# Kernel optimization log

Measured on AMD Instinct MI355X. Metric: run time of the kernel, lower is better.

## Reference

```python
import jax, jax.numpy as jnp
import numpy as np


def _global_field(gi, W1, b1, W2, b2, W3, b3):
    # define_mlp([256,256], global_dim+3, hid_dim, 'ReLU', layer_norm=False)
    h = jax.nn.relu(gi @ W1 + b1)
    h = jax.nn.relu(h @ W2 + b2)
    return h @ W3 + b3  # [..., hid_dim]


def setup_inputs() -> dict:
    key = jax.random.key(0)
    ks = jax.random.split(key, 16)
    B, T, R, P = 4, 4, 512, 32
    G, H = 256, 128
    gin = G + 3  # global_n_freqs is None -> global_in_dim = global_dim + 3
    s = lambda d: 1.0 / np.sqrt(d)
    return {
        'x': jax.random.normal(ks[0], (B, T, R, P, 3), jnp.float32),
        'ray_dir': jax.random.normal(ks[1], (B, T, R, 1, 3), jnp.float32),
        'mask': jax.random.randint(ks[2], (B, T, R, P, 1), 0, 2) == 1,
        'global_feat': jax.random.normal(ks[3], (B, G), jnp.float32),
        'offset': jax.random.normal(ks[4], (B, 3), jnp.float32),
        'local_feat': jax.random.normal(ks[5], (B, T, R, P, H), jnp.float32),
        'W1': jax.random.normal(ks[6], (gin, 256), jnp.float32) * s(gin),
        'b1': jnp.zeros((256,), jnp.float32),
        'W2': jax.random.normal(ks[7], (256, 256), jnp.float32) * s(256),
        'b2': jnp.zeros((256,), jnp.float32),
        'W3': jax.random.normal(ks[8], (256, H), jnp.float32) * s(256),
        'b3': jnp.zeros((H,), jnp.float32),
        'Ws': jax.random.normal(ks[9], (H, 1), jnp.float32) * s(H),
        'bs': jnp.zeros((1,), jnp.float32),
        'Wc': jax.random.normal(ks[10], (H + 3, 3), jnp.float32) * s(H + 3),
        'bc': jnp.zeros((3,), jnp.float32),
    }


def reference(x, ray_dir, mask, global_feat, offset, local_feat,
              W1, b1, W2, b2, W3, b3, Ws, bs, Wc, bc):
    B, T, R, P, _ = x.shape
    m = mask  # [B,T,R,P,1] bool
    # get_global_feat: subtract per-batch offset, gather global_feat per point, concat
    xo = x - offset[:, None, None, None, :]                      # [B,T,R,P,3]
    g = jnp.broadcast_to(global_feat[:, None, None, None, :],
                         (B, T, R, P, global_feat.shape[-1]))    # [B,T,R,P,G]
    gi = jnp.concatenate((g, xo), axis=-1)                       # [B,T,R,P,G+3]
    gfeat = _global_field(gi, W1, b1, W2, b2, W3, b3)            # [B,T,R,P,H]
    # aggregate_shape=False path: feat = aggregated local feat + global feat
    feat = local_feat + gfeat
    # get_shape + shape_act (nerf=True -> softplus(x - 1)), scatter_shape zeros outside mask
    shape = jax.nn.softplus((feat @ Ws + bs) - 1.0)              # [B,T,R,P,1]
    # get_channels on feat + ray_dir, then sigmoid
    rd = jnp.broadcast_to(ray_dir, (B, T, R, P, 3))
    ch = jax.nn.sigmoid(jnp.concatenate((feat, rd), axis=-1) @ Wc + bc)  # [B,T,R,P,3]
    out = jnp.concatenate((shape, ch), axis=-1)
    # dense masked-scatter: valid points keep values, invalid are zero
    return jnp.where(m, out, 0.0)
```

## Files before the change

### kernel.cpp

```cpp
#include <hip/hip_runtime.h>

typedef __attribute__((ext_vector_type(8))) _Float16 f16x8;
typedef __attribute__((ext_vector_type(4))) _Float16 f16x4;
typedef __attribute__((ext_vector_type(4))) float f32x4;

#define SOFF 32768
#define LDS_BYTES (32768 + 4096)
#define NPTS 262144

__device__ inline unsigned swz_h(unsigned row, unsigned colbyte){
  return row*512u + (colbyte ^ ((row & 7u) << 4));
}

__device__ inline f16x8 cvt8(f32x4 a, f32x4 b){
  f16x8 r;
  #pragma unroll
  for (int i = 0; i < 4; ++i){ r[i] = (_Float16)a[i]; r[4+i] = (_Float16)b[i]; }
  return r;
}

__global__ void prep_all(const float* __restrict__ gf, const float* __restrict__ off,
                         const float* __restrict__ W1, const float* __restrict__ b1,
                         const float* __restrict__ W2,
                         const float* __restrict__ W3, const float* __restrict__ b3,
                         const float* __restrict__ Ws, const float* __restrict__ bs,
                         const float* __restrict__ Wc, const float* __restrict__ bc,
                         _Float16* __restrict__ w2t, _Float16* __restrict__ w1h,
                         _Float16* __restrict__ base1h,
                         _Float16* __restrict__ whd, _Float16* __restrict__ wlf,
                         float* __restrict__ hcon, int* __restrict__ counter){
  const int blk = blockIdx.x, tid = threadIdx.x;
  if (blk < 256){
    int e = blk*256 + tid;
    int s = e >> 13, r = e & 8191, n = r >> 5, kk = r & 31;
    w2t[e] = (_Float16)W2[(s*32 + kk)*256 + n];
    if (e < 768){
      int d = e >> 8, j = e & 255;
      w1h[e] = (_Float16)W1[(256 + d)*256 + j];
    }
  } else if (blk < 260){
    int b = blk - 256, j = tid;
    float acc = b1[j];
    for (int k = 0; k < 256; ++k) acc += gf[b*256 + k] * W1[k*256 + j];
    for (int d = 0; d < 3; ++d)  acc -= off[b*3 + d] * W1[(256 + d)*256 + j];
    base1h[b*256 + j] = (_Float16)acc;
  } else {
    int k = tid;
    float s0 = 0.f, s1 = 0.f, s2 = 0.f, s3 = 0.f;
    for (int j = 0; j < 128; ++j){
      float w3 = W3[k*128 + j];
      s0 += w3 * Ws[j];
      s1 += w3 * Wc[j*3 + 0];
      s2 += w3 * Wc[j*3 + 1];
      s3 += w3 * Wc[j*3 + 2];
    }
    int base = (k >> 5)*512 + (k & 31);
    whd[base + 0*32] = (_Float16)s0;
    whd[base + 1*32] = (_Float16)s1;
    whd[base + 2*32] = (_Float16)s2;
    whd[base + 3*32] = (_Float16)s3;
    for (int o = 4; o < 16; ++o) whd[base + o*32] = (_Float16)0.f;
    if (k < 128){
      int bl = (k >> 5)*512 + (k & 31);
      wlf[bl + 0*32] = (_Float16)Ws[k];
      wlf[bl + 1*32] = (_Float16)Wc[k*3 + 0];
      wlf[bl + 2*32] = (_Float16)Wc[k*3 + 1];
      wlf[bl + 3*32] = (_Float16)Wc[k*3 + 2];
      for (int o = 4; o < 16; ++o) wlf[bl + o*32] = (_Float16)0.f;
    }
    if (k == 0){
      float c0 = bs[0], c1 = bc[0], c2 = bc[1], c3 = bc[2];
      for (int j = 0; j < 128; ++j){
        float bj = b3[j];
        c0 += bj * Ws[j];
        c1 += bj * Wc[j*3 + 0];
        c2 += bj * Wc[j*3 + 1];
        c3 += bj * Wc[j*3 + 2];
      }
      hcon[0] = c0; hcon[1] = c1; hcon[2] = c2; hcon[3] = c3;
      *counter = 0;
    }
  }
}

__global__ void compact_mask(const int* __restrict__ mk, int* __restrict__ idx,
                             int* __restrict__ counter, float* __restrict__ out){
  __shared__ int woff[16];
  __shared__ int sbase;
  const int tid = threadIdx.x;
  const int i = blockIdx.x*1024 + tid;
  const int lane = tid & 63, w = tid >> 6;
  int m = (mk[i] != 0);
  unsigned long long bal = __ballot(m);
  if (lane == 0) woff[w] = __popcll(bal);
  __syncthreads();
  if (tid == 0){
    int tot = 0;
    #pragma unroll
    for (int k = 0; k < 16; ++k){ int c = woff[k]; woff[k] = tot; tot += c; }
    sbase = atomicAdd(counter, tot);
  }
  __syncthreads();
  if (m){
    int off = __popcll(bal & ((1ull << lane) - 1ull));
    idx[sbase + woff[w] + off] = i;
  } else {
    *(f32x4*)(out + (size_t)i*4) = (f32x4)0.f;
  }
}

__global__ __launch_bounds__(256, 4) void field_main(
    const float* __restrict__ x, const float* __restrict__ rdv,
    const float* __restrict__ lf, const float* __restrict__ b2v,
    const _Float16* __restrict__ base1h, const _Float16* __restrict__ w1h,
    const _Float16* __restrict__ w2t, const _Float16* __restrict__ whd,
    const _Float16* __restrict__ wlf, const float* __restrict__ hcon,
    const float* __restrict__ Wc, const int* __restrict__ idx,
    const int* __restrict__ nvp, float* __restrict__ out)
{
  const int nv = *nvp;
  const int t0 = blockIdx.x * 64;
  if (t0 >= nv) return;
  const bool full = (t0 + 64 <= nv);

  __shared__ char lds[LDS_BYTES];
  const int tid = threadIdx.x;
  const int wid = tid >> 6, lane = tid & 63;
  const int arow = lane & 15, kgrp = lane >> 4;

  int pi_e = 0; float r0 = 0.f, r1 = 0.f, r2 = 0.f;
  if (tid < 64){
    int ii = t0 + tid; if (ii >= nv) ii = nv - 1;
    pi_e = idx[ii];
    const float* rp = rdv + (pi_e >> 5)*3;
    r0 = rp[0]; r1 = rp[1]; r2 = rp[2];
  }

  const int cw = wid * 64;

  {
    const int j0 = (tid & 31) * 8;
    const int mb = (tid >> 5) * 8;
    f16x8 w0  = *(const f16x8*)(w1h +   0 + j0);
    f16x8 w1v = *(const f16x8*)(w1h + 256 + j0);
    f16x8 w2v = *(const f16x8*)(w1h + 512 + j0);
    const f16x8 z8 = (f16x8)(_Float16)0;
    int pidx[8];
    if (full){
      int4 a = *(const int4*)(idx + t0 + mb);
      int4 b4 = *(const int4*)(idx + t0 + mb + 4);
      pidx[0]=a.x; pidx[1]=a.y; pidx[2]=a.z; pidx[3]=a.w;
      pidx[4]=b4.x; pidx[5]=b4.y; pidx[6]=b4.z; pidx[7]=b4.w;
    } else {
      #pragma unroll
      for (int m = 0; m < 8; ++m){
        int ii = t0 + mb + m; if (ii >= nv) ii = nv - 1;
        pidx[m] = idx[ii];
      }
    }
    #pragma unroll
    for (int m = 0; m < 8; ++m){
      int pi = pidx[m];
      int b  = pi >> 16;
      f16x8 bh = *(const f16x8*)(base1h + b*256 + j0);
      const float* xp = x + (size_t)pi*3;
      _Float16 X0 = (_Float16)xp[0];
      _Float16 X1 = (_Float16)xp[1];
      _Float16 X2 = (_Float16)xp[2];
      f16x8 t = bh;
      t += w0  * X0;
      t += w1v * X1;
      t += w2v * X2;
      t = __builtin_elementwise_max(t, z8);
      *(f16x8*)(lds + swz_h(mb + m, j0*2)) = t;
    }
  }
  __syncthreads();

  f32x4 acc[16];
  #pragma unroll
  for (int c = 0; c < 4; ++c){
    f32x4 bb = *(const f32x4*)(b2v + cw + c*16 + kgrp*4);
    #pragma unroll
    for (int r = 0; r < 4; ++r) acc[r*4+c] = bb;
  }
  #pragma unroll 2
  for (int s = 0; s < 8; ++s){
    f16x8 af[4], bf[4];
    #pragma unroll
    for (int r = 0; r < 4; ++r)
      af[r] = *(const f16x8*)(lds + swz_h(r*16 + arow, s*64 + kgrp*16));
    #pragma unroll
    for (int c = 0; c < 4; ++c)
      bf[c] = *(const f16x8*)(w2t + s*8192 + (cw + c*16 + arow)*32 + kgrp*8);
    __builtin_amdgcn_s_setprio(1);
    #pragma unroll
    for (int r = 0; r < 4; ++r)
      #pragma unroll
      for (int c = 0; c < 4; ++c)
        acc[r*4+c] = __builtin_amdgcn_mfma_f32_16x16x32_f16(bf[c], af[r], acc[r*4+c], 0, 0, 0);
    __builtin_amdgcn_s_setprio(0);
  }

  f32x4 lfa[4], lfb[4];
  #pragma unroll
  for (int c = 0; c < 4; ++c){
    int ii = t0 + c*16 + arow;
    if (!full && ii >= nv) ii = nv - 1;
    int pic = idx[ii];
    const float* lp = lf + (size_t)pic*128 + wid*32 + kgrp*8;
    lfa[c] = *(const f32x4*)lp;
    lfb[c] = *(const f32x4*)(lp + 4);
  }
  __syncthreads();

  #pragma unroll
  for (int r = 0; r < 4; ++r)
    #pragma unroll
    for (int c = 0; c < 4; ++c){
      int row = r*16 + arow;
      int colbyte = (cw + c*16 + kgrp*4) * 2;
      f16x4 v;
      #pragma unroll
      for (int j = 0; j < 4; ++j) v[j] = (_Float16)fmaxf(acc[r*4+c][j], 0.f);
      *(f16x4*)(lds + swz_h(row, colbyte)) = v;
    }

  f32x4 acc4h[4];
  #pragma unroll
  for (int c = 0; c < 4; ++c)
    #pragma unroll
    for (int j = 0; j < 4; ++j)
      acc4h[c][j] = (wid == 0 && kgrp == 0) ? hcon[j] : 0.f;

  #pragma unroll
  for (int s = 0; s < 2; ++s){
    f16x8 ah = *(const f16x8*)(whd + (wid*2 + s)*512 + arow*32 + kgrp*8);
    #pragma unroll
    for (int c = 0; c < 4; ++c){
      f16x8 bh2 = *(const f16x8*)(lds + swz_h(c*16 + arow, (cw + s*32 + kgrp*8)*2));
      acc4h[c] = __builtin_amdgcn_mfma_f32_16x16x32_f16(ah, bh2, acc4h[c], 0, 0, 0);
    }
  }
  {
    f16x8 afl = *(const f16x8*)(wlf + wid*512 + arow*32 + kgrp*8);
    #pragma unroll
    for (int c = 0; c < 4; ++c)
      acc4h[c] = __builtin_amdgcn_mfma_f32_16x16x32_f16(afl, cvt8(lfa[c], lfb[c]), acc4h[c], 0, 0, 0);
  }
  if (kgrp == 0){
    #pragma unroll
    for (int c = 0; c < 4; ++c)
      *(f32x4*)(lds + SOFF + wid*1024 + (c*16 + arow)*16) = acc4h[c];
  }
  __syncthreads();

  if (tid < 64 && t0 + tid < nv){
    f32x4 v = *(const f32x4*)(lds + SOFF + 0*1024 + tid*16);
    #pragma unroll
    for (int w = 1; w < 4; ++w)
      v += *(const f32x4*)(lds + SOFF + w*1024 + tid*16);
    float ps = v[0] - 1.0f;
    float shape = (ps > 20.f) ? ps : log1pf(expf(ps));
    float c0 = v[1] + r0*Wc[128*3+0] + r1*Wc[129*3+0] + r2*Wc[130*3+0];
    float c1 = v[2] + r0*Wc[128*3+1] + r1*Wc[129*3+1] + r2*Wc[130*3+1];
    float c2 = v[3] + r0*Wc[128*3+2] + r1*Wc[129*3+2] + r2*Wc[130*3+2];
    f32x4 o;
    o[0] = shape;
    o[1] = 1.f/(1.f + expf(-c0));
    o[2] = 1.f/(1.f + expf(-c1));
    o[3] = 1.f/(1.f + expf(-c2));
    *(f32x4*)(out + (size_t)pi_e*4) = o;
  }
}

extern "C" void kernel_launch(void* const* d_in, const int* in_sizes, int n_in,
                              void* d_out, int out_size, void* d_ws, size_t ws_size,
                              hipStream_t stream){
  const float* x   = (const float*)d_in[0];
  const float* rd  = (const float*)d_in[1];
  const int*   mk  = (const int*)d_in[2];
  const float* gf  = (const float*)d_in[3];
  const float* off = (const float*)d_in[4];
  const float* lf  = (const float*)d_in[5];
  const float* W1  = (const float*)d_in[6];
  const float* b1  = (const float*)d_in[7];
  const float* W2  = (const float*)d_in[8];
  const float* b2  = (const float*)d_in[9];
  const float* W3  = (const float*)d_in[10];
  const float* b3  = (const float*)d_in[11];
  const float* Ws  = (const float*)d_in[12];
  const float* bs  = (const float*)d_in[13];
  const float* Wc  = (const float*)d_in[14];
  const float* bc  = (const float*)d_in[15];

  char* ws = (char*)d_ws;
  _Float16* base1h = (_Float16*)(ws + 0);
  _Float16* w1h    = (_Float16*)(ws + 2048);
  _Float16* w2t    = (_Float16*)(ws + 4096);
  _Float16* whd    = (_Float16*)(ws + 135168);
  _Float16* wlf    = (_Float16*)(ws + 143360);
  float*    hcon   = (float*)   (ws + 147456);
  int*      counter= (int*)     (ws + 147472);
  int*      idx    = (int*)     (ws + 147520);

  prep_all<<<261, 256, 0, stream>>>(gf, off, W1, b1, W2, W3, b3, Ws, bs, Wc, bc,
                                    w2t, w1h, base1h, whd, wlf, hcon, counter);
  compact_mask<<<NPTS/1024, 1024, 0, stream>>>(mk, idx, counter, (float*)d_out);
  field_main<<<NPTS/64, 256, 0, stream>>>(x, rd, lf, b2,
                                          base1h, w1h, w2t, whd, wlf, hcon, Wc,
                                          idx, counter, (float*)d_out);
}
```

Before: 60.77 us.

## Pack compacted point coords as fp16 with index during mask compaction

```diff
diff --git a/kernel.cpp b/kernel.cpp
--- a/kernel.cpp
+++ b/kernel.cpp
@@ -3,6 +3,7 @@
 typedef __attribute__((ext_vector_type(8))) _Float16 f16x8;
 typedef __attribute__((ext_vector_type(4))) _Float16 f16x4;
 typedef __attribute__((ext_vector_type(4))) float f32x4;
+typedef __attribute__((ext_vector_type(4))) unsigned short u16x4;
 
 #define SOFF 32768
 #define LDS_BYTES (32768 + 4096)
@@ -17,6 +18,14 @@
   #pragma unroll
   for (int i = 0; i < 4; ++i){ r[i] = (_Float16)a[i]; r[4+i] = (_Float16)b[i]; }
   return r;
+}
+
+__device__ inline unsigned short f16bits(float f){
+  _Float16 h = (_Float16)f;
+  return *(unsigned short*)&h;
+}
+__device__ inline _Float16 bits16(unsigned short u){
+  return *(_Float16*)&u;
 }
 
 __global__ void prep_all(const float* __restrict__ gf, const float* __restrict__ off,
@@ -30,16 +39,22 @@
                          _Float16* __restrict__ whd, _Float16* __restrict__ wlf,
                          float* __restrict__ hcon, int* __restrict__ counter){
   const int blk = blockIdx.x, tid = threadIdx.x;
-  if (blk < 256){
-    int e = blk*256 + tid;
-    int s = e >> 13, r = e & 8191, n = r >> 5, kk = r & 31;
-    w2t[e] = (_Float16)W2[(s*32 + kk)*256 + n];
-    if (e < 768){
+  if (blk < 64){
+    #pragma unroll
+    for (int k = 0; k < 4; ++k){
+      int e = blk*1024 + k*256 + tid;
+      int s = e >> 13, r = e & 8191, n = r >> 5, kk = r & 31;
+      w2t[e] = (_Float16)W2[(s*32 + kk)*256 + n];
+    }
+  } else if (blk == 64){
+    #pragma unroll
+    for (int k = 0; k < 3; ++k){
+      int e = k*256 + tid;
       int d = e >> 8, j = e & 255;
       w1h[e] = (_Float16)W1[(256 + d)*256 + j];
     }
-  } else if (blk < 260){
-    int b = blk - 256, j = tid;
+  } else if (blk < 69){
+    int b = blk - 65, j = tid;
     float acc = b1[j];
     for (int k = 0; k < 256; ++k) acc += gf[b*256 + k] * W1[k*256 + j];
     for (int d = 0; d < 3; ++d)  acc -= off[b*3 + d] * W1[(256 + d)*256 + j];
@@ -83,7 +98,8 @@
   }
 }
 
-__global__ void compact_mask(const int* __restrict__ mk, int* __restrict__ idx,
+__global__ void compact_mask(const int* __restrict__ mk, const float* __restrict__ x,
+                             u16x4* __restrict__ px8, unsigned char* __restrict__ pib,
                              int* __restrict__ counter, float* __restrict__ out){
   __shared__ int woff[16];
   __shared__ int sbase;
@@ -103,25 +119,32 @@
   __syncthreads();
   if (m){
     int off = __popcll(bal & ((1ull << lane) - 1ull));
-    idx[sbase + woff[w] + off] = i;
+    int slot = sbase + woff[w] + off;
+    u16x4 r;
+    r[0] = f16bits(x[i*3 + 0]);
+    r[1] = f16bits(x[i*3 + 1]);
+    r[2] = f16bits(x[i*3 + 2]);
+    r[3] = (unsigned short)(i & 0xFFFF);
+    px8[slot] = r;
+    pib[slot] = (unsigned char)(i >> 16);
   } else {
     *(f32x4*)(out + (size_t)i*4) = (f32x4)0.f;
   }
 }
 
 __global__ __launch_bounds__(256, 4) void field_main(
-    const float* __restrict__ x, const float* __restrict__ rdv,
+    const float* __restrict__ rdv,
     const float* __restrict__ lf, const float* __restrict__ b2v,
     const _Float16* __restrict__ base1h, const _Float16* __restrict__ w1h,
     const _Float16* __restrict__ w2t, const _Float16* __restrict__ whd,
     const _Float16* __restrict__ wlf, const float* __restrict__ hcon,
-    const float* __restrict__ Wc, const int* __restrict__ idx,
+    const float* __restrict__ Wc, const u16x4* __restrict__ px8,
+    const unsigned char* __restrict__ pib,
     const int* __restrict__ nvp, float* __restrict__ out)
 {
   const int nv = *nvp;
   const int t0 = blockIdx.x * 64;
   if (t0 >= nv) return;
-  const bool full = (t0 + 64 <= nv);
 
   __shared__ char lds[LDS_BYTES];
   const int tid = threadIdx.x;
@@ -130,8 +153,8 @@
 
   int pi_e = 0; float r0 = 0.f, r1 = 0.f, r2 = 0.f;
   if (tid < 64){
-    int ii = t0 + tid; if (ii >= nv) ii = nv - 1;
-    pi_e = idx[ii];
+    u16x4 px = px8[t0 + tid];
+    pi_e = ((pib[t0 + tid] & 3) << 16) | px[3];
     const float* rp = rdv + (pi_e >> 5)*3;
     r0 = rp[0]; r1 = rp[1]; r2 = rp[2];
   }
@@ -145,28 +168,15 @@
     f16x8 w1v = *(const f16x8*)(w1h + 256 + j0);
     f16x8 w2v = *(const f16x8*)(w1h + 512 + j0);
     const f16x8 z8 = (f16x8)(_Float16)0;
-    int pidx[8];
-    if (full){
-      int4 a = *(const int4*)(idx + t0 + mb);
-      int4 b4 = *(const int4*)(idx + t0 + mb + 4);
-      pidx[0]=a.x; pidx[1]=a.y; pidx[2]=a.z; pidx[3]=a.w;
-      pidx[4]=b4.x; pidx[5]=b4.y; pidx[6]=b4.z; pidx[7]=b4.w;
-    } else {
-      #pragma unroll
-      for (int m = 0; m < 8; ++m){
-        int ii = t0 + mb + m; if (ii >= nv) ii = nv - 1;
-        pidx[m] = idx[ii];
-      }
-    }
     #pragma unroll
     for (int m = 0; m < 8; ++m){
-      int pi = pidx[m];
-      int b  = pi >> 16;
+      int ii = t0 + mb + m;
+      u16x4 px = px8[ii];
+      int b = pib[ii] & 3;
       f16x8 bh = *(const f16x8*)(base1h + b*256 + j0);
-      const float* xp = x + (size_t)pi*3;
-      _Float16 X0 = (_Float16)xp[0];
-      _Float16 X1 = (_Float16)xp[1];
-      _Float16 X2 = (_Float16)xp[2];
+      _Float16 X0 = bits16(px[0]);
+      _Float16 X1 = bits16(px[1]);
+      _Float16 X2 = bits16(px[2]);
       f16x8 t = bh;
       t += w0  * X0;
       t += w1v * X1;
@@ -206,8 +216,7 @@
   #pragma unroll
   for (int c = 0; c < 4; ++c){
     int ii = t0 + c*16 + arow;
-    if (!full && ii >= nv) ii = nv - 1;
-    int pic = idx[ii];
+    int pic = ((pib[ii] & 3) << 16) | px8[ii][3];
     const float* lp = lf + (size_t)pic*128 + wid*32 + kgrp*8;
     lfa[c] = *(const f32x4*)lp;
     lfb[c] = *(const f32x4*)(lp + 4);
@@ -295,19 +304,20 @@
   const float* bc  = (const float*)d_in[15];
 
   char* ws = (char*)d_ws;
-  _Float16* base1h = (_Float16*)(ws + 0);
-  _Float16* w1h    = (_Float16*)(ws + 2048);
-  _Float16* w2t    = (_Float16*)(ws + 4096);
-  _Float16* whd    = (_Float16*)(ws + 135168);
-  _Float16* wlf    = (_Float16*)(ws + 143360);
-  float*    hcon   = (float*)   (ws + 147456);
-  int*      counter= (int*)     (ws + 147472);
-  int*      idx    = (int*)     (ws + 147520);
-
-  prep_all<<<261, 256, 0, stream>>>(gf, off, W1, b1, W2, W3, b3, Ws, bs, Wc, bc,
-                                    w2t, w1h, base1h, whd, wlf, hcon, counter);
-  compact_mask<<<NPTS/1024, 1024, 0, stream>>>(mk, idx, counter, (float*)d_out);
-  field_main<<<NPTS/64, 256, 0, stream>>>(x, rd, lf, b2,
+  _Float16* base1h    = (_Float16*)(ws + 0);
+  _Float16* w1h       = (_Float16*)(ws + 2048);
+  _Float16* w2t       = (_Float16*)(ws + 4096);
+  _Float16* whd       = (_Float16*)(ws + 135168);
+  _Float16* wlf       = (_Float16*)(ws + 143360);
+  float*    hcon      = (float*)   (ws + 147456);
+  int*      counter   = (int*)     (ws + 147472);
+  u16x4*    px8       = (u16x4*)   (ws + 147712);
+  unsigned char* pib  = (unsigned char*)(ws + 147712 + NPTS*8);
+
+  prep_all<<<70, 256, 0, stream>>>(gf, off, W1, b1, W2, W3, b3, Ws, bs, Wc, bc,
+                                   w2t, w1h, base1h, whd, wlf, hcon, counter);
+  compact_mask<<<NPTS/1024, 1024, 0, stream>>>(mk, x, px8, pib, counter, (float*)d_out);
+  field_main<<<NPTS/64, 256, 0, stream>>>(rd, lf, b2,
                                           base1h, w1h, w2t, whd, wlf, hcon, Wc,
-                                          idx, counter, (float*)d_out);
-}
+                                          px8, pib, counter, (float*)d_out);
+}
```

New measurement: 59.51 us. 2.1% less time.
